# Kernel optimization log

Hardware: AMD Instinct MI355X
Metric: run time of the kernel (lower is better)

The kernel has to match this reference:

```python
import jax, jax.numpy as jnp
import numpy as np

B, S, D = 4, 2048, 1024

def setup_inputs() -> dict:
    key = jax.random.key(0)
    ks = jax.random.split(key, 7)
    sc = 1.0 / np.sqrt(D)
    return {
        "x": jax.random.normal(ks[0], (B, S, D), dtype=jnp.float32),
        "Wq": jax.random.normal(ks[1], (D, D), dtype=jnp.float32) * sc,
        "bq": jax.random.normal(ks[2], (D,), dtype=jnp.float32) * 0.01,
        "Wk": jax.random.normal(ks[3], (D, D), dtype=jnp.float32) * sc,
        "bk": jax.random.normal(ks[4], (D,), dtype=jnp.float32) * 0.01,
        "Wv": jax.random.normal(ks[5], (D, D), dtype=jnp.float32) * sc,
        "bv": jax.random.normal(ks[6], (D,), dtype=jnp.float32) * 0.01,
    }

def reference(x, Wq, bq, Wk, bk, Wv, bv):
    # q, k, v: [B, S, D] projections (torch Linear: x @ W^T + b; here W stored as [in, out])
    q = jnp.einsum("bsd,df->bsf", x, Wq) + bq
    k = jnp.einsum("bsd,df->bsf", x, Wk) + bk
    v = jnp.einsum("bsd,df->bsf", x, Wv) + bv
    dim = x.shape[-1]
    # scores: [B, S, S], scaled by sqrt(full d_model) as in the source
    scores = jnp.einsum("bqd,bkd->bqk", q, k) / jnp.sqrt(jnp.float32(dim)).astype(x.dtype)
    attn = jax.nn.softmax(scores, axis=-1)
    return jnp.einsum("bqk,bkd->bqd", attn, v)
```

## Files before the change

### kernel.cpp

```cpp
#include <hip/hip_runtime.h>
#include <hip/hip_bf16.h>

typedef __attribute__((ext_vector_type(8))) short bf16x8;
typedef __attribute__((ext_vector_type(4))) float f32x4;
typedef unsigned short u16;

__device__ __forceinline__ u16 f2bf(float f) {
  unsigned int u = __builtin_bit_cast(unsigned int, f);
  u += 0x7fffu + ((u >> 16) & 1u);
  return (u16)(u >> 16);
}

__device__ __forceinline__ void gload_lds16(const void* g, void* l) {
  __builtin_amdgcn_global_load_lds(
      (const __attribute__((address_space(1))) void*)g,
      (__attribute__((address_space(3))) void*)l, 16, 0, 0);
}

#define BAR() __builtin_amdgcn_s_barrier()
#define VMC(N) asm volatile("s_waitcnt vmcnt(%0)" ::"n"(N) : "memory")

template <int EPI>
__global__ __launch_bounds__(256) void gemm2s(
    const u16* __restrict__ Abase, const u16* __restrict__ Btbase,
    const float* __restrict__ p0, const float* __restrict__ p1,
    const float* __restrict__ p2, void* __restrict__ out0,
    void* __restrict__ out1, int Kd, int Kext, int ldc, long long sAz,
    long long sBz, long long sCz) {
  constexpr int ASZ = 16384;
  constexpr int BSZ = 16384;
  constexpr int BBASE = 2 * ASZ;
  __shared__ char lds[2 * ASZ + 3 * BSZ];

  const int tid = threadIdx.x;
  const int w = tid >> 6, l = tid & 63;
  const int wr = w >> 1, wc = w & 1;
  const int lq = l >> 4, lr = l & 15;
  const int bm = blockIdx.y * 128, bn = blockIdx.x * 128;
  const int z = blockIdx.z;
  const u16* A = Abase + (size_t)z * sAz;
  const u16* Bt = Btbase + (size_t)z * sBz;
  const int NT = Kext >> 6;

  const int kbp = ((tid & 7) ^ ((tid >> 3) & 7)) * 8;
  const int drow = tid >> 3;
  const u16* gA[4];
  const u16* gB[4];
#pragma unroll
  for (int u = 0; u < 4; ++u) {
    gA[u] = A + (size_t)(bm + u * 32 + drow) * Kd + kbp;
    gB[u] = Bt + (size_t)(bn + u * 32 + drow) * Kd + kbp;
  }

  auto stageA = [&](int kt) {
    char* d = lds + (kt & 1) * ASZ + tid * 16;
#pragma unroll
    for (int u = 0; u < 4; ++u) gload_lds16(gA[u] + kt * 64, d + u * 4096);
  };
  auto stageB = [&](int kt) {
    char* d = lds + BBASE + (kt % 3) * BSZ + tid * 16;
#pragma unroll
    for (int u = 0; u < 4; ++u) gload_lds16(gB[u] + kt * 64, d + u * 4096);
  };

  const int rA = wr * 64 + lr;
  const int rB0 = wc * 64 + lr;
  int aoff[2];
#pragma unroll
  for (int kh = 0; kh < 2; ++kh)
    aoff[kh] = rA * 128 + (((kh * 4 + lq) ^ (rA & 7)) << 4);

  f32x4 acc[4][2][2] = {};
  bf16x8 a[2][4];
  bf16x8 bb[2][2][2];

  auto rdA = [&](int kt) {
    const char* p = lds + (kt & 1) * ASZ;
#pragma unroll
    for (int kh = 0; kh < 2; ++kh)
#pragma unroll
      for (int mf = 0; mf < 4; ++mf)
        a[kh][mf] = *(const bf16x8*)(p + aoff[kh] + mf * 2048);
  };
  auto rdB = [&](int kt) {
    const char* p = lds + BBASE + (kt % 3) * BSZ;
#pragma unroll
    for (int nh = 0; nh < 2; ++nh) {
      const int rB = rB0 + nh * 32;
#pragma unroll
      for (int kh = 0; kh < 2; ++kh) {
        const int o = rB * 128 + (((kh * 4 + lq) ^ (rB & 7)) << 4);
#pragma unroll
        for (int nf = 0; nf < 2; ++nf)
          bb[nh][kh][nf] = *(const bf16x8*)(p + o + nf * 2048);
      }
    }
  };
  auto mma = [&](int kh) {
    __builtin_amdgcn_s_setprio(1);
#pragma unroll
    for (int nh = 0; nh < 2; ++nh)
#pragma unroll
      for (int mf = 0; mf < 4; ++mf)
#pragma unroll
        for (int nf = 0; nf < 2; ++nf)
          acc[mf][nh][nf] = __builtin_amdgcn_mfma_f32_16x16x32_bf16(
              a[kh][mf], bb[nh][kh][nf], acc[mf][nh][nf], 0, 0, 0);
    __builtin_amdgcn_s_setprio(0);
  };

  stageB(0);
  stageA(0);
  stageB(1);
  stageA(1);
  VMC(8);
  BAR();

  for (int t = 0; t < NT; ++t) {
    rdA(t);
    rdB(t);
    if (t + 2 < NT) stageB(t + 2);
    BAR();
    mma(0);
    if (t + 2 < NT) VMC(4); else VMC(0);
    BAR();
    if (t + 2 < NT) stageA(t + 2);
    mma(1);
  }

  if constexpr (EPI == 4) {
    u16* C = (u16*)out0 + (size_t)z * sCz;
    const float* cc = p0 + z * 2048;
    float* rs = (float*)p1 + z * 2048;
    float psum[4][4] = {};
#pragma unroll
    for (int nh = 0; nh < 2; ++nh)
#pragma unroll
      for (int nf = 0; nf < 2; ++nf) {
        const int col = bn + wc * 64 + nh * 32 + nf * 16 + lr;
        const float cj = cc[col];
#pragma unroll
        for (int mf = 0; mf < 4; ++mf) {
          const int row = bm + wr * 64 + mf * 16 + lq * 4;
#pragma unroll
          for (int e = 0; e < 4; ++e) {
            const float pv = __expf((acc[mf][nh][nf][e] + cj) * 0.03125f);
            C[(size_t)(row + e) * ldc + col] = f2bf(pv);
            psum[mf][e] += pv;
          }
        }
      }
#pragma unroll
    for (int off = 1; off <= 8; off <<= 1)
#pragma unroll
      for (int mf = 0; mf < 4; ++mf)
#pragma unroll
        for (int e = 0; e < 4; ++e)
          psum[mf][e] += __shfl_xor(psum[mf][e], off, 64);
    if (lr == 0) {
#pragma unroll
      for (int mf = 0; mf < 4; ++mf)
#pragma unroll
        for (int e = 0; e < 4; ++e)
          atomicAdd(&rs[bm + wr * 64 + mf * 16 + lq * 4 + e], psum[mf][e]);
    }
  } else if constexpr (EPI == 5) {
    float* C = (float*)out0 + (size_t)z * sCz;
    const float* rs = p0 + z * 2048;
#pragma unroll
    for (int nh = 0; nh < 2; ++nh)
#pragma unroll
      for (int nf = 0; nf < 2; ++nf) {
        const int col = bn + wc * 64 + nh * 32 + nf * 16 + lr;
#pragma unroll
        for (int mf = 0; mf < 4; ++mf) {
          const int row = bm + wr * 64 + mf * 16 + lq * 4;
#pragma unroll
          for (int e = 0; e < 4; ++e)
            C[(size_t)(row + e) * ldc + col] =
                acc[mf][nh][nf][e] / rs[row + e];
        }
      }
  } else if constexpr (EPI == 6) {
    float* C = (float*)out0 + (size_t)z * sCz;
#pragma unroll
    for (int nh = 0; nh < 2; ++nh)
#pragma unroll
      for (int nf = 0; nf < 2; ++nf) {
        const int col = bn + wc * 64 + nh * 32 + nf * 16 + lr;
#pragma unroll
        for (int mf = 0; mf < 4; ++mf) {
          const int row = bm + wr * 64 + mf * 16 + lq * 4;
#pragma unroll
          for (int e = 0; e < 4; ++e)
            C[(size_t)(row + e) * ldc + col] = acc[mf][nh][nf][e];
        }
      }
  } else {
    const int mat = bn >> 10;
    u16* T = (u16*)out0;
    u16* V = (u16*)out1;
#pragma unroll
    for (int nh = 0; nh < 2; ++nh)
#pragma unroll
      for (int nf = 0; nf < 2; ++nf) {
        const int oc = (bn + wc * 64 + nh * 32 + nf * 16 + lr) & 1023;
        if (mat == 0) {
#pragma unroll
          for (int mf = 0; mf < 4; ++mf) {
            const int row = bm + wr * 64 + mf * 16 + lq * 4;
#pragma unroll
            for (int e = 0; e < 4; ++e)
              T[(size_t)(row + e) * 1024 + oc] = f2bf(acc[mf][nh][nf][e]);
          }
        } else {
          const float bb2 = p2[oc];
#pragma unroll
          for (int mf = 0; mf < 4; ++mf) {
            const int row = bm + wr * 64 + mf * 16 + lq * 4;
            const int bz = row >> 11, sdx = row & 2047;
            ushort4 pk;
            pk.x = f2bf(acc[mf][nh][nf][0] + bb2);
            pk.y = f2bf(acc[mf][nh][nf][1] + bb2);
            pk.z = f2bf(acc[mf][nh][nf][2] + bb2);
            pk.w = f2bf(acc[mf][nh][nf][3] + bb2);
            *(ushort4*)&V[((size_t)bz * 1024 + oc) * 2048 + sdx] = pk;
          }
        }
      }
  }
}

__global__ __launch_bounds__(256) void cvt_x(const float* __restrict__ in,
                                             u16* __restrict__ out) {
  const int i = blockIdx.x * 256 + threadIdx.x;
  const float4 v = ((const float4*)in)[i];
  ushort4 o;
  o.x = f2bf(v.x);
  o.y = f2bf(v.y);
  o.z = f2bf(v.z);
  o.w = f2bf(v.w);
  ((ushort4*)out)[i] = o;
}

__global__ void cvt_w3(const float* __restrict__ Wq,
                       const float* __restrict__ Wk,
                       const float* __restrict__ Wv, u16* __restrict__ Wqb,
                       u16* __restrict__ Wkb, u16* __restrict__ WtTV) {
  __shared__ float s[32][33];
  const int tx = threadIdx.x, ty = threadIdx.y;
  const int k0 = blockIdx.y * 32, n0 = blockIdx.x * 32;
  if (blockIdx.z == 2) {
    s[ty][tx] = Wv[(size_t)(k0 + ty) * 1024 + n0 + tx];
    __syncthreads();
    WtTV[1048576 + (size_t)(n0 + ty) * 1024 + k0 + tx] = f2bf(s[tx][ty]);
  } else {
    const float* W = blockIdx.z ? Wk : Wq;
    u16* O = blockIdx.z ? Wkb : Wqb;
    const size_t i = (size_t)(k0 + ty) * 1024 + n0 + tx;
    O[i] = f2bf(W[i]);
  }
}

__global__ __launch_bounds__(256) void mcast(const float* __restrict__ Mf,
                                             u16* __restrict__ Mt) {
  const int i = blockIdx.x * 256 + threadIdx.x;
  const float4 a = ((const float4*)Mf)[i];
  const float4 b = ((const float4*)(Mf + 1048576))[i];
  const float4 c = ((const float4*)(Mf + 2097152))[i];
  const float4 d = ((const float4*)(Mf + 3145728))[i];
  ushort4 o;
  o.x = f2bf(a.x + b.x + c.x + d.x);
  o.y = f2bf(a.y + b.y + c.y + d.y);
  o.z = f2bf(a.z + b.z + c.z + d.z);
  o.w = f2bf(a.w + b.w + c.w + d.w);
  ((ushort4*)Mt)[i] = o;
}

__global__ __launch_bounds__(256) void vker(const float* __restrict__ Wk,
                                            const float* __restrict__ bq,
                                            float* __restrict__ v) {
  const int d = blockIdx.x, t = threadIdx.x;
  const float4 wv = ((const float4*)(Wk + (size_t)d * 1024))[t];
  const float4 bv = ((const float4*)bq)[t];
  float p = wv.x * bv.x + wv.y * bv.y + wv.z * bv.z + wv.w * bv.w;
#pragma unroll
  for (int o = 32; o; o >>= 1) p += __shfl_xor(p, o, 64);
  __shared__ float red[4];
  if ((t & 63) == 0) red[t >> 6] = p;
  __syncthreads();
  if (t == 0) v[d] = red[0] + red[1] + red[2] + red[3];
}

__global__ __launch_bounds__(256) void cker(const float* __restrict__ x,
                                            const float* __restrict__ v,
                                            float* __restrict__ c) {
  const int j = blockIdx.x * 8 + (threadIdx.x >> 5);
  const int lane = threadIdx.x & 31;
  const float* xr = x + (size_t)j * 1024;
  float p = 0.f;
#pragma unroll
  for (int k = 0; k < 8; ++k) {
    const int i4 = k * 32 + lane;
    const float4 xv = ((const float4*)xr)[i4];
    const float4 vv = ((const float4*)v)[i4];
    p += xv.x * vv.x + xv.y * vv.y + xv.z * vv.z + xv.w * vv.w;
  }
#pragma unroll
  for (int o = 16; o; o >>= 1) p += __shfl_xor(p, o, 64);
  if (lane == 0) c[j] = p;
}

extern "C" void kernel_launch(void* const* d_in, const int* in_sizes, int n_in,
                              void* d_out, int out_size, void* d_ws,
                              size_t ws_size, hipStream_t stream) {
  const float* x = (const float*)d_in[0];
  const float* Wq = (const float*)d_in[1];
  const float* bq = (const float*)d_in[2];
  const float* Wk = (const float*)d_in[3];
  const float* bv = (const float*)d_in[6];
  const float* Wv = (const float*)d_in[5];
  float* out = (float*)d_out;
  char* ws = (char*)d_ws;

  u16* xb = (u16*)ws;
  u16* WtTV = (u16*)(ws + 16777216);
  u16* Wqb = (u16*)(ws + 20971520);
  u16* Wkb = (u16*)(ws + 23068672);
  float* vvec = (float*)(ws + 25165824);
  float* cvec = (float*)(ws + 25169920);
  float* rowsum = (float*)(ws + 25202688);
  float* Mf32 = (float*)(ws + 25235456);
  u16* T = (u16*)(ws + 25235456);
  u16* Vt = (u16*)(ws + 42012672);
  u16* SP = (u16*)(ws + 58789888);

  hipMemsetAsync(rowsum, 0, 32768, stream);

  cvt_x<<<8192, 256, 0, stream>>>(x, xb);
  cvt_w3<<<dim3(32, 32, 3), dim3(32, 32), 0, stream>>>(Wq, Wk, Wv, Wqb, Wkb,
                                                       WtTV);
  vker<<<1024, 256, 0, stream>>>(Wk, bq, vvec);
  cker<<<1024, 256, 0, stream>>>(x, vvec, cvec);

  gemm2s<6><<<dim3(8, 8, 4), 256, 0, stream>>>(
      Wkb, Wqb, nullptr, nullptr, nullptr, Mf32, nullptr, 1024, 256, 1024,
      256LL, 256LL, 1048576LL);
  mcast<<<1024, 256, 0, stream>>>(Mf32, WtTV);

  gemm2s<7><<<dim3(16, 64, 1), 256, 0, stream>>>(
      xb, WtTV, nullptr, nullptr, bv, T, Vt, 1024, 1024, 0, 0, 0, 0);

  gemm2s<4><<<dim3(16, 16, 4), 256, 0, stream>>>(
      T, xb, cvec, rowsum, nullptr, SP, nullptr, 1024, 1024, 2048, 2097152LL,
      2097152LL, 4194304LL);

  gemm2s<5><<<dim3(8, 16, 4), 256, 0, stream>>>(
      SP, Vt, rowsum, nullptr, nullptr, out, nullptr, 2048, 2048, 1024,
      4194304LL, 2097152LL, 2097152LL);
}
```

Before: 181.3 us.

## Widen main GEMM tiles to 128x256 with 8 waves per block

The three large GEMMs move to a new kernel using 512-thread blocks, 4x2 wave layout, and a 128x256 output tile, with a larger B staging buffer. The small M-precompute GEMM is split into its own 256-thread kernel without the priority hints. Wider tiles raise reuse of A per loaded byte and halve the block count. In exchange LDS usage grows to about 128KB per block and the launch bounds request 2 blocks per CU, which may not fit and could lower occupancy. The grid shrinks, which may leave CUs underfilled.

```diff
diff --git a/kernel.cpp b/kernel.cpp
--- a/kernel.cpp
+++ b/kernel.cpp
@@ -21,46 +21,47 @@
 #define VMC(N) asm volatile("s_waitcnt vmcnt(%0)" ::"n"(N) : "memory")
 
 template <int EPI>
-__global__ __launch_bounds__(256) void gemm2s(
+__global__ __launch_bounds__(512, 2) void gemm2t(
     const u16* __restrict__ Abase, const u16* __restrict__ Btbase,
-    const float* __restrict__ p0, const float* __restrict__ p1,
+    const float* __restrict__ p0, float* __restrict__ p1,
     const float* __restrict__ p2, void* __restrict__ out0,
-    void* __restrict__ out1, int Kd, int Kext, int ldc, long long sAz,
-    long long sBz, long long sCz) {
+    void* __restrict__ out1, int Kd, int ldc, long long sAz, long long sBz,
+    long long sCz) {
   constexpr int ASZ = 16384;
-  constexpr int BSZ = 16384;
+  constexpr int BSZ = 32768;
   constexpr int BBASE = 2 * ASZ;
   __shared__ char lds[2 * ASZ + 3 * BSZ];
 
   const int tid = threadIdx.x;
   const int w = tid >> 6, l = tid & 63;
-  const int wr = w >> 1, wc = w & 1;
+  const int wr = w >> 2, wc = w & 3;
   const int lq = l >> 4, lr = l & 15;
-  const int bm = blockIdx.y * 128, bn = blockIdx.x * 128;
+  const int bm = blockIdx.y * 128, bn = blockIdx.x * 256;
   const int z = blockIdx.z;
   const u16* A = Abase + (size_t)z * sAz;
   const u16* Bt = Btbase + (size_t)z * sBz;
-  const int NT = Kext >> 6;
+  const int NT = Kd >> 6;
 
   const int kbp = ((tid & 7) ^ ((tid >> 3) & 7)) * 8;
   const int drow = tid >> 3;
-  const u16* gA[4];
+  const u16* gA[2];
   const u16* gB[4];
 #pragma unroll
-  for (int u = 0; u < 4; ++u) {
-    gA[u] = A + (size_t)(bm + u * 32 + drow) * Kd + kbp;
-    gB[u] = Bt + (size_t)(bn + u * 32 + drow) * Kd + kbp;
-  }
+  for (int u = 0; u < 2; ++u)
+    gA[u] = A + (size_t)(bm + u * 64 + drow) * Kd + kbp;
+#pragma unroll
+  for (int u = 0; u < 4; ++u)
+    gB[u] = Bt + (size_t)(bn + u * 64 + drow) * Kd + kbp;
 
   auto stageA = [&](int kt) {
     char* d = lds + (kt & 1) * ASZ + tid * 16;
 #pragma unroll
-    for (int u = 0; u < 4; ++u) gload_lds16(gA[u] + kt * 64, d + u * 4096);
+    for (int u = 0; u < 2; ++u) gload_lds16(gA[u] + kt * 64, d + u * 8192);
   };
   auto stageB = [&](int kt) {
     char* d = lds + BBASE + (kt % 3) * BSZ + tid * 16;
 #pragma unroll
-    for (int u = 0; u < 4; ++u) gload_lds16(gB[u] + kt * 64, d + u * 4096);
+    for (int u = 0; u < 4; ++u) gload_lds16(gB[u] + kt * 64, d + u * 8192);
   };
 
   const int rA = wr * 64 + lr;
@@ -113,7 +114,7 @@
   stageA(0);
   stageB(1);
   stageA(1);
-  VMC(8);
+  VMC(6);
   BAR();
 
   for (int t = 0; t < NT; ++t) {
@@ -131,7 +132,7 @@
   if constexpr (EPI == 4) {
     u16* C = (u16*)out0 + (size_t)z * sCz;
     const float* cc = p0 + z * 2048;
-    float* rs = (float*)p1 + z * 2048;
+    float* rs = p1 + z * 2048;
     float psum[4][4] = {};
 #pragma unroll
     for (int nh = 0; nh < 2; ++nh)
@@ -166,7 +167,7 @@
     }
   } else if constexpr (EPI == 5) {
     float* C = (float*)out0 + (size_t)z * sCz;
-    const float* rs = p0 + z * 2048;
+    const float* rs = p1 + z * 2048;
 #pragma unroll
     for (int nh = 0; nh < 2; ++nh)
 #pragma unroll
@@ -179,21 +180,6 @@
           for (int e = 0; e < 4; ++e)
             C[(size_t)(row + e) * ldc + col] =
                 acc[mf][nh][nf][e] / rs[row + e];
-        }
-      }
-  } else if constexpr (EPI == 6) {
-    float* C = (float*)out0 + (size_t)z * sCz;
-#pragma unroll
-    for (int nh = 0; nh < 2; ++nh)
-#pragma unroll
-      for (int nf = 0; nf < 2; ++nf) {
-        const int col = bn + wc * 64 + nh * 32 + nf * 16 + lr;
-#pragma unroll
-        for (int mf = 0; mf < 4; ++mf) {
-          const int row = bm + wr * 64 + mf * 16 + lq * 4;
-#pragma unroll
-          for (int e = 0; e < 4; ++e)
-            C[(size_t)(row + e) * ldc + col] = acc[mf][nh][nf][e];
         }
       }
   } else {
@@ -229,6 +215,125 @@
         }
       }
   }
+}
+
+__global__ __launch_bounds__(256) void gemmM(
+    const u16* __restrict__ Abase, const u16* __restrict__ Btbase,
+    float* __restrict__ out0, int Kd, int Kext, int ldc, long long sAz,
+    long long sBz, long long sCz) {
+  constexpr int ASZ = 16384;
+  constexpr int BSZ = 16384;
+  constexpr int BBASE = 2 * ASZ;
+  __shared__ char lds[2 * ASZ + 3 * BSZ];
+
+  const int tid = threadIdx.x;
+  const int w = tid >> 6, l = tid & 63;
+  const int wr = w >> 1, wc = w & 1;
+  const int lq = l >> 4, lr = l & 15;
+  const int bm = blockIdx.y * 128, bn = blockIdx.x * 128;
+  const int z = blockIdx.z;
+  const u16* A = Abase + (size_t)z * sAz;
+  const u16* Bt = Btbase + (size_t)z * sBz;
+  const int NT = Kext >> 6;
+
+  const int kbp = ((tid & 7) ^ ((tid >> 3) & 7)) * 8;
+  const int drow = tid >> 3;
+  const u16* gA[4];
+  const u16* gB[4];
+#pragma unroll
+  for (int u = 0; u < 4; ++u) {
+    gA[u] = A + (size_t)(bm + u * 32 + drow) * Kd + kbp;
+    gB[u] = Bt + (size_t)(bn + u * 32 + drow) * Kd + kbp;
+  }
+
+  auto stageA = [&](int kt) {
+    char* d = lds + (kt & 1) * ASZ + tid * 16;
+#pragma unroll
+    for (int u = 0; u < 4; ++u) gload_lds16(gA[u] + kt * 64, d + u * 4096);
+  };
+  auto stageB = [&](int kt) {
+    char* d = lds + BBASE + (kt % 3) * BSZ + tid * 16;
+#pragma unroll
+    for (int u = 0; u < 4; ++u) gload_lds16(gB[u] + kt * 64, d + u * 4096);
+  };
+
+  const int rA = wr * 64 + lr;
+  const int rB0 = wc * 64 + lr;
+  int aoff[2];
+#pragma unroll
+  for (int kh = 0; kh < 2; ++kh)
+    aoff[kh] = rA * 128 + (((kh * 4 + lq) ^ (rA & 7)) << 4);
+
+  f32x4 acc[4][2][2] = {};
+  bf16x8 a[2][4];
+  bf16x8 bb[2][2][2];
+
+  auto rdA = [&](int kt) {
+    const char* p = lds + (kt & 1) * ASZ;
+#pragma unroll
+    for (int kh = 0; kh < 2; ++kh)
+#pragma unroll
+      for (int mf = 0; mf < 4; ++mf)
+        a[kh][mf] = *(const bf16x8*)(p + aoff[kh] + mf * 2048);
+  };
+  auto rdB = [&](int kt) {
+    const char* p = lds + BBASE + (kt % 3) * BSZ;
+#pragma unroll
+    for (int nh = 0; nh < 2; ++nh) {
+      const int rB = rB0 + nh * 32;
+#pragma unroll
+      for (int kh = 0; kh < 2; ++kh) {
+        const int o = rB * 128 + (((kh * 4 + lq) ^ (rB & 7)) << 4);
+#pragma unroll
+        for (int nf = 0; nf < 2; ++nf)
+          bb[nh][kh][nf] = *(const bf16x8*)(p + o + nf * 2048);
+      }
+    }
+  };
+  auto mma = [&](int kh) {
+#pragma unroll
+    for (int nh = 0; nh < 2; ++nh)
+#pragma unroll
+      for (int mf = 0; mf < 4; ++mf)
+#pragma unroll
+        for (int nf = 0; nf < 2; ++nf)
+          acc[mf][nh][nf] = __builtin_amdgcn_mfma_f32_16x16x32_bf16(
+              a[kh][mf], bb[nh][kh][nf], acc[mf][nh][nf], 0, 0, 0);
+  };
+
+  stageB(0);
+  stageA(0);
+  stageB(1);
+  stageA(1);
+  VMC(8);
+  BAR();
+
+  for (int t = 0; t < NT; ++t) {
+    rdA(t);
+    rdB(t);
+    if (t + 2 < NT) stageB(t + 2);
+    BAR();
+    mma(0);
+    if (t + 2 < NT) VMC(4); else VMC(0);
+    BAR();
+    if (t + 2 < NT) stageA(t + 2);
+    mma(1);
+  }
+
+  float* C = out0 + (size_t)z * sCz;
+#pragma unroll
+  for (int nh = 0; nh < 2; ++nh)
+#pragma unroll
+    for (int nf = 0; nf < 2; ++nf) {
+      const int col = bn + wc * 64 + nh * 32 + nf * 16 + lr;
+#pragma unroll
+      for (int mf = 0; mf < 4; ++mf) {
+        const int row = bm + wr * 64 + mf * 16 + lq * 4;
+#pragma unroll
+        for (int e = 0; e < 4; ++e)
+          C[(size_t)(row + e) * ldc + col] = acc[mf][nh][nf][e];
+      }
+    }
 }
 
 __global__ __launch_bounds__(256) void cvt_x(const float* __restrict__ in,
@@ -318,8 +423,8 @@
   const float* Wq = (const float*)d_in[1];
   const float* bq = (const float*)d_in[2];
   const float* Wk = (const float*)d_in[3];
+  const float* Wv = (const float*)d_in[5];
   const float* bv = (const float*)d_in[6];
-  const float* Wv = (const float*)d_in[5];
   float* out = (float*)d_out;
   char* ws = (char*)d_ws;
 
@@ -343,19 +448,18 @@
   vker<<<1024, 256, 0, stream>>>(Wk, bq, vvec);
   cker<<<1024, 256, 0, stream>>>(x, vvec, cvec);
 
-  gemm2s<6><<<dim3(8, 8, 4), 256, 0, stream>>>(
-      Wkb, Wqb, nullptr, nullptr, nullptr, Mf32, nullptr, 1024, 256, 1024,
-      256LL, 256LL, 1048576LL);
+  gemmM<<<dim3(8, 8, 4), 256, 0, stream>>>(Wkb, Wqb, Mf32, 1024, 256, 1024,
+                                           256LL, 256LL, 1048576LL);
   mcast<<<1024, 256, 0, stream>>>(Mf32, WtTV);
 
-  gemm2s<7><<<dim3(16, 64, 1), 256, 0, stream>>>(
-      xb, WtTV, nullptr, nullptr, bv, T, Vt, 1024, 1024, 0, 0, 0, 0);
-
-  gemm2s<4><<<dim3(16, 16, 4), 256, 0, stream>>>(
-      T, xb, cvec, rowsum, nullptr, SP, nullptr, 1024, 1024, 2048, 2097152LL,
+  gemm2t<7><<<dim3(8, 64, 1), 512, 0, stream>>>(
+      xb, WtTV, nullptr, nullptr, bv, T, Vt, 1024, 0, 0, 0, 0);
+
+  gemm2t<4><<<dim3(8, 16, 4), 512, 0, stream>>>(
+      T, xb, cvec, rowsum, nullptr, SP, nullptr, 1024, 2048, 2097152LL,
       2097152LL, 4194304LL);
 
-  gemm2s<5><<<dim3(8, 16, 4), 256, 0, stream>>>(
-      SP, Vt, rowsum, nullptr, nullptr, out, nullptr, 2048, 2048, 1024,
-      4194304LL, 2097152LL, 2097152LL);
-}
+  gemm2t<5><<<dim3(4, 16, 4), 512, 0, stream>>>(
+      SP, Vt, nullptr, rowsum, nullptr, out, nullptr, 2048, 1024, 4194304LL,
+      2097152LL, 2097152LL);
+}
```

Result: faster. 177.5 us (-2.1%).
